# Kernel tuning notes

Hardware: AMD Instinct MI355X
Metric: run time of the kernel (lower is better)

## Reference

```python
import jax, jax.numpy as jnp
import numpy as np

L, D, DH, NH, P = 12, 768, 64, 12, 16
B, H_IMG, W_IMG = 16, 384, 384
MAX_GRID = 64


def setup_inputs() -> dict:
    key = jax.random.key(0)
    ks = jax.random.split(key, 10)
    r = lambda k, shp: (0.02 * jax.random.normal(k, shp, dtype=jnp.float32))
    return {
        "x": jax.random.normal(ks[0], (B, 3, H_IMG, W_IMG), dtype=jnp.float32),
        "conv_w": r(ks[1], (D, 3, P, P)),
        "conv_b": jnp.zeros((D,), jnp.float32),
        "ln_w": jnp.ones((D,), jnp.float32),
        "ln_b": jnp.zeros((D,), jnp.float32),
        "pos_y_emb": r(ks[2], (MAX_GRID, D)),
        "pos_x_emb": r(ks[3], (MAX_GRID, D)),
        "mha_ln_w": jnp.ones((L, D), jnp.float32),
        "mha_ln_b": jnp.zeros((L, D), jnp.float32),
        "qw": r(ks[4], (L, D, D)),
        "kw": r(ks[5], (L, D, D)),
        "vw": r(ks[6], (L, D, D)),
        "ffn_ln_w": jnp.ones((L, D), jnp.float32),
        "ffn_ln_b": jnp.zeros((L, D), jnp.float32),
        "w1": r(ks[7], (L, D, 4 * D)),
        "b1": jnp.zeros((L, 4 * D), jnp.float32),
        "w2": r(ks[8], (L, 4 * D, D)),
        "b2": jnp.zeros((L, D), jnp.float32),
        "x_shift": 0,
        "y_shift": 0,
    }


def _ln(x, w, b):
    m = jnp.mean(x, axis=-1, keepdims=True)
    v = jnp.var(x, axis=-1, keepdims=True)
    return (x - m) * jax.lax.rsqrt(v + 1e-5) * w + b


def reference(x, conv_w, conv_b, ln_w, ln_b, pos_y_emb, pos_x_emb,
              mha_ln_w, mha_ln_b, qw, kw, vw,
              ffn_ln_w, ffn_ln_b, w1, b1, w2, b2, x_shift, y_shift):
    # patch embed: conv + relu, to NHWC, layernorm
    h = jax.lax.conv_general_dilated(x, conv_w, (P, P), 'VALID',
                                     dimension_numbers=('NCHW', 'OIHW', 'NCHW'))
    h = jax.nn.relu(h + conv_b[None, :, None, None])
    h = jnp.transpose(h, (0, 2, 3, 1))  # [B, GH, GW, D]
    h = _ln(h, ln_w, ln_b)
    b, gh, gw, d = h.shape
    n = gh * gw
    # 2D factorized positional embedding, shared layernorm
    pos = (pos_y_emb[jnp.arange(gh) + y_shift][:, None, :]
           + pos_x_emb[jnp.arange(gw) + x_shift][None, :, :])  # [GH, GW, D]
    pos = _ln(pos, ln_w, ln_b).reshape(1, n, d)
    pos_emb = jnp.broadcast_to(pos, (b, n, d))
    t = h.reshape(b, n, d) + pos_emb
    scale = 1.0 / jnp.sqrt(jnp.float32(DH))
    for i in range(L):
        # pre-LN MHA (no output projection, mask=None / pretrain=False)
        tl = _ln(t, mha_ln_w[i], mha_ln_b[i])
        q = (tl @ qw[i]).reshape(b, n, NH, DH).transpose(0, 2, 1, 3)
        k = (tl @ kw[i]).reshape(b, n, NH, DH).transpose(0, 2, 1, 3)
        v = (tl @ vw[i]).reshape(b, n, NH, DH).transpose(0, 2, 1, 3)
        attn = jax.nn.softmax(jnp.einsum('bhqd,bhkd->bhqk', q, k) * scale, axis=-1)
        o = jnp.einsum('bhqk,bhkd->bhqd', attn, v).transpose(0, 2, 1, 3).reshape(b, n, d)
        t = t + o
        fl = _ln(t, ffn_ln_w[i], ffn_ln_b[i])
        t = t + (jax.nn.relu(fl @ w1[i] + b1[i]) @ w2[i] + b2[i])
    return t, pos_emb
```

## Files before the change

### kernel.cpp

```cpp
#include <hip/hip_runtime.h>

typedef unsigned short u16;
typedef __attribute__((ext_vector_type(4))) float f32x4;
typedef __attribute__((ext_vector_type(8))) short s16x8;

__device__ __forceinline__ u16 f2bf(float f) {
    union { float f; unsigned u; } v; v.f = f;
    unsigned r = v.u + 0x7FFFu + ((v.u >> 16) & 1u);
    return (u16)(r >> 16);
}

__device__ __forceinline__ void gload_lds16(const u16* g, u16* l) {
    __builtin_amdgcn_global_load_lds(
        (const __attribute__((address_space(1))) unsigned int*)(g),
        (__attribute__((address_space(3))) unsigned int*)(l),
        16, 0, 0);
}

#define NTOK 9216
#define SEQ  576
#define DMODEL 768
#define DFF  3072
#define NHEAD 12
#define HDIM 64

__global__ __launch_bounds__(256) void convert_bf16_kernel(const float* __restrict__ in,
                                                           u16* __restrict__ out, int n) {
    for (int i = blockIdx.x * 256 + threadIdx.x; i < n; i += gridDim.x * 256)
        out[i] = f2bf(in[i]);
}

__global__ __launch_bounds__(256) void copy_f32_kernel(const float* __restrict__ in,
                                                       float* __restrict__ out, int n4) {
    const float4* a = (const float4*)in;
    float4* o = (float4*)out;
    for (int i = blockIdx.x * 256 + threadIdx.x; i < n4; i += gridDim.x * 256)
        o[i] = a[i];
}

__global__ __launch_bounds__(256) void im2col_kernel(const float* __restrict__ x,
                                                     u16* __restrict__ out) {
    int tok = blockIdx.x;
    int b = tok / SEQ, n = tok % SEQ;
    int gy = n / 24, gx = n % 24;
    int tid = threadIdx.x;
#pragma unroll
    for (int j = 0; j < 3; ++j) {
        int col = tid + j * 256;
        int c = col >> 8, py = (col >> 4) & 15, px = col & 15;
        float v = x[(size_t)((b * 3 + c) * 384 + gy * 16 + py) * 384 + gx * 16 + px];
        out[(size_t)tok * DMODEL + col] = f2bf(v);
    }
}

__global__ __launch_bounds__(256) void transpose_layer_kernel(
        const float* __restrict__ qw, const float* __restrict__ kw, const float* __restrict__ vw,
        const float* __restrict__ w1, const float* __restrict__ w2,
        u16* __restrict__ wTq, u16* __restrict__ wTk, u16* __restrict__ wTv,
        u16* __restrict__ w1T, u16* __restrict__ w2T) {
    int bid = blockIdx.x;
    const float* src; u16* dst; int Kd, Nd, tile;
    if (bid < 1728)      { int m = bid / 576; src = m == 0 ? qw : (m == 1 ? kw : vw);
                           dst = m == 0 ? wTq : (m == 1 ? wTk : wTv); Kd = 768; Nd = 768; tile = bid % 576; }
    else if (bid < 4032) { src = w1; dst = w1T; Kd = 768; Nd = 3072; tile = bid - 1728; }
    else                 { src = w2; dst = w2T; Kd = 3072; Nd = 768; tile = bid - 4032; }
    int ntx = Nd / 32;
    int tk = (tile / ntx) * 32, tn = (tile % ntx) * 32;
    __shared__ float ts[32][33];
    int tx = threadIdx.x & 31, ty = threadIdx.x >> 5;
#pragma unroll
    for (int j = 0; j < 32; j += 8)
        ts[ty + j][tx] = src[(size_t)(tk + ty + j) * Nd + tn + tx];
    __syncthreads();
#pragma unroll
    for (int j = 0; j < 32; j += 8)
        dst[(size_t)(tn + ty + j) * Kd + tk + tx] = f2bf(ts[tx][ty + j]);
}

__global__ __launch_bounds__(256) void ln_bf16_kernel(const float* __restrict__ X,
                                                      const float* __restrict__ w,
                                                      const float* __restrict__ b,
                                                      u16* __restrict__ Y) {
    int row = blockIdx.x, tid = threadIdx.x;
    const float* x = X + (size_t)row * DMODEL;
    float v0 = x[tid], v1 = x[tid + 256], v2 = x[tid + 512];
    float s = v0 + v1 + v2, sq = v0 * v0 + v1 * v1 + v2 * v2;
#pragma unroll
    for (int off = 32; off >= 1; off >>= 1) { s += __shfl_down(s, off); sq += __shfl_down(sq, off); }
    __shared__ float red[8];
    if ((tid & 63) == 0) { red[tid >> 6] = s; red[4 + (tid >> 6)] = sq; }
    __syncthreads();
    float S = red[0] + red[1] + red[2] + red[3];
    float Q = red[4] + red[5] + red[6] + red[7];
    float mean = S * (1.f / DMODEL);
    float var = Q * (1.f / DMODEL) - mean * mean;
    float inv = rsqrtf(var + 1e-5f);
    u16* y = Y + (size_t)row * DMODEL;
    y[tid]       = f2bf((v0 - mean) * inv * w[tid]       + b[tid]);
    y[tid + 256] = f2bf((v1 - mean) * inv * w[tid + 256] + b[tid + 256]);
    y[tid + 512] = f2bf((v2 - mean) * inv * w[tid + 512] + b[tid + 512]);
}

__global__ __launch_bounds__(256) void ln_add_pos_kernel(float* __restrict__ T,
                                                         const float* __restrict__ w,
                                                         const float* __restrict__ b,
                                                         const float* __restrict__ posln) {
    int row = blockIdx.x, tid = threadIdx.x;
    float* x = T + (size_t)row * DMODEL;
    const float* p = posln + (size_t)(row % SEQ) * DMODEL;
    float v0 = x[tid], v1 = x[tid + 256], v2 = x[tid + 512];
    float s = v0 + v1 + v2, sq = v0 * v0 + v1 * v1 + v2 * v2;
#pragma unroll
    for (int off = 32; off >= 1; off >>= 1) { s += __shfl_down(s, off); sq += __shfl_down(sq, off); }
    __shared__ float red[8];
    if ((tid & 63) == 0) { red[tid >> 6] = s; red[4 + (tid >> 6)] = sq; }
    __syncthreads();
    float S = red[0] + red[1] + red[2] + red[3];
    float Q = red[4] + red[5] + red[6] + red[7];
    float mean = S * (1.f / DMODEL);
    float var = Q * (1.f / DMODEL) - mean * mean;
    float inv = rsqrtf(var + 1e-5f);
    x[tid]       = (v0 - mean) * inv * w[tid]       + b[tid]       + p[tid];
    x[tid + 256] = (v1 - mean) * inv * w[tid + 256] + b[tid + 256] + p[tid + 256];
    x[tid + 512] = (v2 - mean) * inv * w[tid + 512] + b[tid + 512] + p[tid + 512];
}

__global__ __launch_bounds__(256) void pos_ln_kernel(const float* __restrict__ py,
                                                     const float* __restrict__ px,
                                                     const float* __restrict__ w,
                                                     const float* __restrict__ b,
                                                     const int* __restrict__ xs_p,
                                                     const int* __restrict__ ys_p,
                                                     float* __restrict__ posln,
                                                     float* __restrict__ out2) {
    int row = blockIdx.x;
    int gy = row / 24, gx = row % 24;
    int ys = ys_p[0], xs = xs_p[0];
    int tid = threadIdx.x;
    float v[3]; float s = 0.f, sq = 0.f;
#pragma unroll
    for (int j = 0; j < 3; ++j) {
        int c = tid + j * 256;
        v[j] = py[(size_t)(gy + ys) * DMODEL + c] + px[(size_t)(gx + xs) * DMODEL + c];
        s += v[j]; sq += v[j] * v[j];
    }
#pragma unroll
    for (int off = 32; off >= 1; off >>= 1) { s += __shfl_down(s, off); sq += __shfl_down(sq, off); }
    __shared__ float red[8];
    if ((tid & 63) == 0) { red[tid >> 6] = s; red[4 + (tid >> 6)] = sq; }
    __syncthreads();
    float S = red[0] + red[1] + red[2] + red[3];
    float Q = red[4] + red[5] + red[6] + red[7];
    float mean = S * (1.f / DMODEL);
    float var = Q * (1.f / DMODEL) - mean * mean;
    float inv = rsqrtf(var + 1e-5f);
#pragma unroll
    for (int j = 0; j < 3; ++j) {
        int c = tid + j * 256;
        float y = (v[j] - mean) * inv * w[c] + b[c];
        posln[(size_t)row * DMODEL + c] = y;
        for (int bb = 0; bb < 16; ++bb)
            out2[((size_t)bb * SEQ + row) * DMODEL + c] = y;
    }
}

#define EPI_CONV 0
#define EPI_QKV  1
#define EPI_FFN1 3
#define EPI_FFN2 4

template <int EPI>
__global__ __launch_bounds__(256, 3) void gemm4w(const u16* __restrict__ A,
                                                 const u16* __restrict__ Bt,
                                                 float* __restrict__ outF,
                                                 u16* __restrict__ outB,
                                                 u16* __restrict__ outB2,
                                                 u16* __restrict__ outB3,
                                                 const float* __restrict__ bias,
                                                 int lda, int N, int K) {
    __shared__ __align__(16) u16 lds[3 * 8192];
    const int tid = threadIdx.x;
    const int wave = tid >> 6, lane = tid & 63;
    const int c_lo = lane & 15, c_hi = lane >> 4;
    const int wm = wave >> 1, wn = wave & 1;
    const int m0 = blockIdx.x * 128, n0 = blockIdx.y * 128;
    const int NT = K >> 5;

    const int srow = tid >> 2;
    const int koff = ((tid & 3) * 8) ^ (((tid >> 3) & 3) << 3);
    const u16* pA0 = A  + (size_t)(m0 + srow) * lda + koff;
    const u16* pA1 = pA0 + (size_t)64 * lda;
    const u16* pB0 = Bt + (size_t)(n0 + srow) * lda + koff;
    const u16* pB1 = pB0 + (size_t)64 * lda;
    f32x4 acc[4][4] = {};

    auto stage = [&](int t) {
        u16* buf = lds + (t % 3) * 8192;
        int k0 = t << 5;
        gload_lds16(pA0 + k0, buf + tid * 8);
        gload_lds16(pA1 + k0, buf + 2048 + tid * 8);
        gload_lds16(pB0 + k0, buf + 4096 + tid * 8);
        gload_lds16(pB1 + k0, buf + 6144 + tid * 8);
    };

    stage(0); stage(1);
    asm volatile("s_waitcnt vmcnt(4)" ::: "memory");
    __builtin_amdgcn_s_barrier();
    __builtin_amdgcn_sched_barrier(0);

    const int colA = (c_hi * 8) ^ (((c_lo >> 1) & 3) << 3);

    for (int t = 0; t < NT; ++t) {
        if (t + 2 < NT) stage(t + 2);
        const u16* buf = lds + (t % 3) * 8192;
        s16x8 af[4], bf[4];
#pragma unroll
        for (int m = 0; m < 4; ++m)
            af[m] = *(const s16x8*)(buf + (wm * 64 + m * 16 + c_lo) * 32 + colA);
#pragma unroll
        for (int n = 0; n < 4; ++n)
            bf[n] = *(const s16x8*)(buf + 4096 + (wn * 64 + n * 16 + c_lo) * 32 + colA);
        asm volatile("s_waitcnt lgkmcnt(0)" ::: "memory");
        __builtin_amdgcn_sched_barrier(0);
        __builtin_amdgcn_s_setprio(1);
#pragma unroll
        for (int m = 0; m < 4; ++m)
#pragma unroll
            for (int n = 0; n < 4; ++n)
                acc[m][n] = __builtin_amdgcn_mfma_f32_16x16x32_bf16(af[m], bf[n], acc[m][n], 0, 0, 0);
        __builtin_amdgcn_s_setprio(0);
        if (t + 2 < NT)      { asm volatile("s_waitcnt vmcnt(4)" ::: "memory"); }
        else if (t + 1 < NT) { asm volatile("s_waitcnt vmcnt(0)" ::: "memory"); }
        __builtin_amdgcn_s_barrier();
        __builtin_amdgcn_sched_barrier(0);
    }

#pragma unroll
    for (int mf = 0; mf < 4; ++mf)
#pragma unroll
        for (int nf = 0; nf < 4; ++nf)
#pragma unroll
            for (int rr = 0; rr < 4; ++rr) {
                int grow = m0 + wm * 64 + mf * 16 + c_hi * 4 + rr;
                int gcol = n0 + wn * 64 + nf * 16 + c_lo;
                float v = acc[mf][nf][rr];
                if (EPI == EPI_CONV) {
                    v += bias[gcol]; v = fmaxf(v, 0.f);
                    outF[(size_t)grow * 768 + gcol] = v;
                } else if (EPI == EPI_QKV) {
                    int sel = n0 / 768;
                    int lcol = gcol - sel * 768;
                    if (sel == 0)      outB [(size_t)grow * 768 + lcol] = f2bf(v);
                    else if (sel == 1) outB2[(size_t)grow * 768 + lcol] = f2bf(v);
                    else {
                        int b = grow / SEQ, nt = grow % SEQ;
                        int h = lcol >> 6, dh = lcol & 63;
                        outB3[(size_t)(((b * NHEAD + h) << 6) + dh) * SEQ + nt] = f2bf(v);
                    }
                } else if (EPI == EPI_FFN1) {
                    v += bias[gcol]; v = fmaxf(v, 0.f);
                    outB[(size_t)grow * N + gcol] = f2bf(v);
                } else if (EPI == EPI_FFN2) {
                    outF[(size_t)grow * 768 + gcol] += v + bias[gcol];
                }
            }
}

__global__ __launch_bounds__(256) void attn_kernel(const u16* __restrict__ Qb,
                                                   const u16* __restrict__ Kb,
                                                   const u16* __restrict__ Vt,
                                                   float* __restrict__ T) {
    int bid = blockIdx.x;
    int qt = bid / 192, bh = bid % 192;
    int b = bh / NHEAD, h = bh % NHEAD;
    int q0 = qt * 64;
    const int tid = threadIdx.x, wave = tid >> 6, lane = tid & 63;
    const int c_lo = lane & 15, c_hi = lane >> 4;
    __shared__ __align__(16) u16 Qs[64][72];
    __shared__ __align__(16) u16 Ks[64][72];
    __shared__ __align__(16) u16 Vs[64][72];
    __shared__ __align__(16) u16 Ps[4][16][72];
#pragma unroll
    for (int i = 0; i < 2; ++i) {
        int c = i * 256 + tid, row = c >> 3, slot = (c & 7) * 8;
        *(s16x8*)&Qs[row][slot] =
            *(const s16x8*)(Qb + ((size_t)(b * SEQ + q0 + row) * DMODEL + h * HDIM + slot));
    }
    s16x8 kreg[2], vreg[2];
    {
#pragma unroll
        for (int i = 0; i < 2; ++i) {
            int c = i * 256 + tid, row = c >> 3, slot = (c & 7) * 8;
            kreg[i] = *(const s16x8*)(Kb + ((size_t)(b * SEQ + row) * DMODEL + h * HDIM + slot));
            vreg[i] = *(const s16x8*)(Vt + ((size_t)((b * NHEAD + h) * HDIM + row) * SEQ + slot));
        }
    }
    f32x4 o[4] = {};
    float mrun[4], lrun[4];
#pragma unroll
    for (int r = 0; r < 4; ++r) { mrun[r] = -1e30f; lrun[r] = 0.f; }
    for (int t2 = 0; t2 < 9; ++t2) {
        __builtin_amdgcn_s_barrier();
#pragma unroll
        for (int i = 0; i < 2; ++i) {
            int c = i * 256 + tid, row = c >> 3, slot = (c & 7) * 8;
            *(s16x8*)&Ks[row][slot] = kreg[i];
            *(s16x8*)&Vs[row][slot] = vreg[i];
        }
        asm volatile("s_waitcnt lgkmcnt(0)" ::: "memory");
        __builtin_amdgcn_s_barrier();
        __builtin_amdgcn_sched_barrier(0);
        if (t2 < 8) {
            int kv0 = (t2 + 1) * 64;
#pragma unroll
            for (int i = 0; i < 2; ++i) {
                int c = i * 256 + tid, row = c >> 3, slot = (c & 7) * 8;
                kreg[i] = *(const s16x8*)(Kb + ((size_t)(b * SEQ + kv0 + row) * DMODEL + h * HDIM + slot));
                vreg[i] = *(const s16x8*)(Vt + ((size_t)((b * NHEAD + h) * HDIM + row) * SEQ + kv0 + slot));
            }
        }
        f32x4 s[4] = {};
        s16x8 aq[2];
#pragma unroll
        for (int ks = 0; ks < 2; ++ks)
            aq[ks] = *(const s16x8*)&Qs[wave * 16 + c_lo][ks * 32 + c_hi * 8];
#pragma unroll
        for (int nf = 0; nf < 4; ++nf)
#pragma unroll
            for (int ks = 0; ks < 2; ++ks) {
                s16x8 bk = *(const s16x8*)&Ks[nf * 16 + c_lo][ks * 32 + c_hi * 8];
                s[nf] = __builtin_amdgcn_mfma_f32_16x16x32_bf16(aq[ks], bk, s[nf], 0, 0, 0);
            }
#pragma unroll
        for (int nf = 0; nf < 4; ++nf)
#pragma unroll
            for (int r = 0; r < 4; ++r) s[nf][r] *= 0.125f;
        float mx[4];
#pragma unroll
        for (int r = 0; r < 4; ++r)
            mx[r] = fmaxf(fmaxf(s[0][r], s[1][r]), fmaxf(s[2][r], s[3][r]));
#pragma unroll
        for (int off = 1; off < 16; off <<= 1)
#pragma unroll
            for (int r = 0; r < 4; ++r) mx[r] = fmaxf(mx[r], __shfl_xor(mx[r], off));
        float alpha[4];
#pragma unroll
        for (int r = 0; r < 4; ++r) {
            float mn = fmaxf(mrun[r], mx[r]);
            alpha[r] = __expf(mrun[r] - mn);
            mrun[r] = mn;
            lrun[r] *= alpha[r];
        }
        float ls[4] = {0.f, 0.f, 0.f, 0.f};
        u16 pb[4][4];
#pragma unroll
        for (int nf = 0; nf < 4; ++nf)
#pragma unroll
            for (int r = 0; r < 4; ++r) {
                float p = __expf(s[nf][r] - mrun[r]);
                ls[r] += p;
                pb[nf][r] = f2bf(p);
            }
#pragma unroll
        for (int off = 1; off < 16; off <<= 1)
#pragma unroll
            for (int r = 0; r < 4; ++r) ls[r] += __shfl_xor(ls[r], off);
#pragma unroll
        for (int r = 0; r < 4; ++r) lrun[r] += ls[r];
#pragma unroll
        for (int df = 0; df < 4; ++df)
#pragma unroll
            for (int r = 0; r < 4; ++r) o[df][r] *= alpha[r];
#pragma unroll
        for (int nf = 0; nf < 4; ++nf)
#pragma unroll
            for (int r = 0; r < 4; ++r)
                Ps[wave][c_hi * 4 + r][c_lo + nf * 16] = pb[nf][r];
        asm volatile("s_waitcnt lgkmcnt(0)" ::: "memory");
        s16x8 pa[2];
#pragma unroll
        for (int ks = 0; ks < 2; ++ks)
            pa[ks] = *(const s16x8*)&Ps[wave][c_lo][ks * 32 + c_hi * 8];
#pragma unroll
        for (int df = 0; df < 4; ++df)
#pragma unroll
            for (int ks = 0; ks < 2; ++ks) {
                s16x8 bv = *(const s16x8*)&Vs[df * 16 + c_lo][ks * 32 + c_hi * 8];
                o[df] = __builtin_amdgcn_mfma_f32_16x16x32_bf16(pa[ks], bv, o[df], 0, 0, 0);
            }
    }
#pragma unroll
    for (int df = 0; df < 4; ++df)
#pragma unroll
        for (int r = 0; r < 4; ++r) {
            int grow = b * SEQ + q0 + wave * 16 + c_hi * 4 + r;
            int gcol = h * HDIM + df * 16 + c_lo;
            T[(size_t)grow * DMODEL + gcol] += o[df][r] / lrun[r];
        }
}

extern "C" void kernel_launch(void* const* d_in, const int* in_sizes, int n_in,
                              void* d_out, int out_size, void* d_ws, size_t ws_size,
                              hipStream_t stream) {
    (void)in_sizes; (void)n_in; (void)out_size; (void)ws_size;
    const float* x        = (const float*)d_in[0];
    const float* conv_w   = (const float*)d_in[1];
    const float* conv_b   = (const float*)d_in[2];
    const float* ln_w     = (const float*)d_in[3];
    const float* ln_b     = (const float*)d_in[4];
    const float* pos_y    = (const float*)d_in[5];
    const float* pos_x    = (const float*)d_in[6];
    const float* mha_ln_w = (const float*)d_in[7];
    const float* mha_ln_b = (const float*)d_in[8];
    const float* qw       = (const float*)d_in[9];
    const float* kw       = (const float*)d_in[10];
    const float* vw       = (const float*)d_in[11];
    const float* ffn_ln_w = (const float*)d_in[12];
    const float* ffn_ln_b = (const float*)d_in[13];
    const float* w1       = (const float*)d_in[14];
    const float* b1       = (const float*)d_in[15];
    const float* w2       = (const float*)d_in[16];
    const float* b2       = (const float*)d_in[17];
    const int*   xs       = (const int*)d_in[18];
    const int*   ys       = (const int*)d_in[19];
    float* out1 = (float*)d_out;
    float* out2 = out1 + (size_t)NTOK * DMODEL;

    size_t off = 0;
    char* ws = (char*)d_ws;
    auto carve = [&](size_t bytes) { char* p = ws + off; off += (bytes + 255) & ~(size_t)255; return p; };
    u16* wTqkv = (u16*)carve((size_t)3 * 768 * 768 * 2);
    u16* w1T = (u16*)carve((size_t)DFF * DMODEL * 2);
    u16* w2T = (u16*)carve((size_t)DMODEL * DFF * 2);
    float* t  = (float*)carve((size_t)NTOK * DMODEL * 4);
    u16* tl   = (u16*)carve((size_t)NTOK * DMODEL * 2);
    u16* qb   = (u16*)carve((size_t)NTOK * DMODEL * 2);
    u16* kb   = (u16*)carve((size_t)NTOK * DMODEL * 2);
    u16* vT   = (u16*)carve((size_t)NTOK * DMODEL * 2);
    u16* hb   = (u16*)carve((size_t)NTOK * DFF * 2);
    float* posln = (float*)carve((size_t)SEQ * DMODEL * 4);
    u16* wTq = wTqkv;
    u16* wTk = wTqkv + (size_t)768 * 768;
    u16* wTv = wTqkv + (size_t)2 * 768 * 768;
    u16* cw   = wTqkv;
    u16* im2c = hb;

    convert_bf16_kernel<<<1152, 256, 0, stream>>>(conv_w, cw, 768 * 768);
    im2col_kernel<<<NTOK, 256, 0, stream>>>(x, im2c);
    gemm4w<EPI_CONV><<<dim3(72, 6), 256, 0, stream>>>(im2c, cw, t, nullptr, nullptr, nullptr,
                                                      conv_b, 768, 768, 768);
    pos_ln_kernel<<<SEQ, 256, 0, stream>>>(pos_y, pos_x, ln_w, ln_b, xs, ys, posln, out2);
    ln_add_pos_kernel<<<NTOK, 256, 0, stream>>>(t, ln_w, ln_b, posln);

    for (int i = 0; i < 12; ++i) {
        transpose_layer_kernel<<<6336, 256, 0, stream>>>(
            qw + (size_t)i * 768 * 768, kw + (size_t)i * 768 * 768, vw + (size_t)i * 768 * 768,
            w1 + (size_t)i * 768 * DFF, w2 + (size_t)i * DFF * 768,
            wTq, wTk, wTv, w1T, w2T);
        ln_bf16_kernel<<<NTOK, 256, 0, stream>>>(t, mha_ln_w + i * DMODEL, mha_ln_b + i * DMODEL, tl);
        gemm4w<EPI_QKV><<<dim3(72, 18), 256, 0, stream>>>(tl, wTqkv, nullptr, qb, kb, vT,
                                                          nullptr, 768, 2304, 768);
        attn_kernel<<<16 * NHEAD * 9, 256, 0, stream>>>(qb, kb, vT, t);
        ln_bf16_kernel<<<NTOK, 256, 0, stream>>>(t, ffn_ln_w + i * DMODEL, ffn_ln_b + i * DMODEL, tl);
        gemm4w<EPI_FFN1><<<dim3(72, 24), 256, 0, stream>>>(tl, w1T, nullptr, hb, nullptr, nullptr,
                                                           b1 + (size_t)i * DFF, 768, 3072, 768);
        gemm4w<EPI_FFN2><<<dim3(72, 6), 256, 0, stream>>>(hb, w2T, t, nullptr, nullptr, nullptr,
                                                          b2 + (size_t)i * DMODEL, 3072, 768, 3072);
    }
    copy_f32_kernel<<<2048, 256, 0, stream>>>(t, out1, (NTOK * DMODEL) / 4);
}
```

Before: 3.260 ms.

## Single-buffer GEMM main loop and use 64x64 vectorized weight transpose

```diff
diff --git a/kernel.cpp b/kernel.cpp
--- a/kernel.cpp
+++ b/kernel.cpp
@@ -53,28 +53,38 @@
     }
 }
 
-__global__ __launch_bounds__(256) void transpose_layer_kernel(
+__global__ __launch_bounds__(256) void transpose64_kernel(
         const float* __restrict__ qw, const float* __restrict__ kw, const float* __restrict__ vw,
         const float* __restrict__ w1, const float* __restrict__ w2,
         u16* __restrict__ wTq, u16* __restrict__ wTk, u16* __restrict__ wTv,
         u16* __restrict__ w1T, u16* __restrict__ w2T) {
     int bid = blockIdx.x;
     const float* src; u16* dst; int Kd, Nd, tile;
-    if (bid < 1728)      { int m = bid / 576; src = m == 0 ? qw : (m == 1 ? kw : vw);
-                           dst = m == 0 ? wTq : (m == 1 ? wTk : wTv); Kd = 768; Nd = 768; tile = bid % 576; }
-    else if (bid < 4032) { src = w1; dst = w1T; Kd = 768; Nd = 3072; tile = bid - 1728; }
-    else                 { src = w2; dst = w2T; Kd = 3072; Nd = 768; tile = bid - 4032; }
-    int ntx = Nd / 32;
-    int tk = (tile / ntx) * 32, tn = (tile % ntx) * 32;
-    __shared__ float ts[32][33];
-    int tx = threadIdx.x & 31, ty = threadIdx.x >> 5;
-#pragma unroll
-    for (int j = 0; j < 32; j += 8)
-        ts[ty + j][tx] = src[(size_t)(tk + ty + j) * Nd + tn + tx];
+    if (bid < 432)       { int m = bid / 144; src = m == 0 ? qw : (m == 1 ? kw : vw);
+                           dst = m == 0 ? wTq : (m == 1 ? wTk : wTv); Kd = 768; Nd = 768; tile = bid % 144; }
+    else if (bid < 1008) { src = w1; dst = w1T; Kd = 768; Nd = 3072; tile = bid - 432; }
+    else                 { src = w2; dst = w2T; Kd = 3072; Nd = 768; tile = bid - 1008; }
+    int ntx = Nd >> 6;
+    int tk = (tile / ntx) << 6, tn = (tile % ntx) << 6;
+    __shared__ float ts[64][65];
+    int tx4 = threadIdx.x & 15, ty = threadIdx.x >> 4;
+#pragma unroll
+    for (int j = 0; j < 64; j += 16) {
+        float4 v = *(const float4*)&src[(size_t)(tk + ty + j) * Nd + tn + tx4 * 4];
+        ts[ty + j][tx4 * 4 + 0] = v.x;
+        ts[ty + j][tx4 * 4 + 1] = v.y;
+        ts[ty + j][tx4 * 4 + 2] = v.z;
+        ts[ty + j][tx4 * 4 + 3] = v.w;
+    }
     __syncthreads();
-#pragma unroll
-    for (int j = 0; j < 32; j += 8)
-        dst[(size_t)(tn + ty + j) * Kd + tk + tx] = f2bf(ts[tx][ty + j]);
+    int kx = threadIdx.x & 31, ry = threadIdx.x >> 5;
+#pragma unroll
+    for (int j = 0; j < 64; j += 8) {
+        int r = ry + j;
+        unsigned lo = f2bf(ts[2 * kx][r]);
+        unsigned hi = f2bf(ts[2 * kx + 1][r]);
+        *(unsigned*)&dst[(size_t)(tn + r) * Kd + tk + 2 * kx] = lo | (hi << 16);
+    }
 }
 
 __global__ __launch_bounds__(256) void ln_bf16_kernel(const float* __restrict__ X,
@@ -170,7 +180,7 @@
 #define EPI_FFN2 4
 
 template <int EPI>
-__global__ __launch_bounds__(256, 3) void gemm4w(const u16* __restrict__ A,
+__global__ __launch_bounds__(256, 3) void gemm97(const u16* __restrict__ A,
                                                  const u16* __restrict__ Bt,
                                                  float* __restrict__ outF,
                                                  u16* __restrict__ outB,
@@ -178,7 +188,7 @@
                                                  u16* __restrict__ outB3,
                                                  const float* __restrict__ bias,
                                                  int lda, int N, int K) {
-    __shared__ __align__(16) u16 lds[3 * 8192];
+    __shared__ __align__(16) u16 lds[8192];
     const int tid = threadIdx.x;
     const int wave = tid >> 6, lane = tid & 63;
     const int c_lo = lane & 15, c_hi = lane >> 4;
@@ -194,45 +204,28 @@
     const u16* pB1 = pB0 + (size_t)64 * lda;
     f32x4 acc[4][4] = {};
 
-    auto stage = [&](int t) {
-        u16* buf = lds + (t % 3) * 8192;
+    const int colA = (c_hi * 8) ^ (((c_lo >> 1) & 3) << 3);
+
+    for (int t = 0; t < NT; ++t) {
         int k0 = t << 5;
-        gload_lds16(pA0 + k0, buf + tid * 8);
-        gload_lds16(pA1 + k0, buf + 2048 + tid * 8);
-        gload_lds16(pB0 + k0, buf + 4096 + tid * 8);
-        gload_lds16(pB1 + k0, buf + 6144 + tid * 8);
-    };
-
-    stage(0); stage(1);
-    asm volatile("s_waitcnt vmcnt(4)" ::: "memory");
-    __builtin_amdgcn_s_barrier();
-    __builtin_amdgcn_sched_barrier(0);
-
-    const int colA = (c_hi * 8) ^ (((c_lo >> 1) & 3) << 3);
-
-    for (int t = 0; t < NT; ++t) {
-        if (t + 2 < NT) stage(t + 2);
-        const u16* buf = lds + (t % 3) * 8192;
+        __syncthreads();
+        gload_lds16(pA0 + k0, lds + tid * 8);
+        gload_lds16(pA1 + k0, lds + 2048 + tid * 8);
+        gload_lds16(pB0 + k0, lds + 4096 + tid * 8);
+        gload_lds16(pB1 + k0, lds + 6144 + tid * 8);
+        __syncthreads();
         s16x8 af[4], bf[4];
 #pragma unroll
         for (int m = 0; m < 4; ++m)
-            af[m] = *(const s16x8*)(buf + (wm * 64 + m * 16 + c_lo) * 32 + colA);
+            af[m] = *(const s16x8*)(lds + (wm * 64 + m * 16 + c_lo) * 32 + colA);
 #pragma unroll
         for (int n = 0; n < 4; ++n)
-            bf[n] = *(const s16x8*)(buf + 4096 + (wn * 64 + n * 16 + c_lo) * 32 + colA);
-        asm volatile("s_waitcnt lgkmcnt(0)" ::: "memory");
-        __builtin_amdgcn_sched_barrier(0);
-        __builtin_amdgcn_s_setprio(1);
+            bf[n] = *(const s16x8*)(lds + 4096 + (wn * 64 + n * 16 + c_lo) * 32 + colA);
 #pragma unroll
         for (int m = 0; m < 4; ++m)
 #pragma unroll
             for (int n = 0; n < 4; ++n)
                 acc[m][n] = __builtin_amdgcn_mfma_f32_16x16x32_bf16(af[m], bf[n], acc[m][n], 0, 0, 0);
-        __builtin_amdgcn_s_setprio(0);
-        if (t + 2 < NT)      { asm volatile("s_waitcnt vmcnt(4)" ::: "memory"); }
-        else if (t + 1 < NT) { asm volatile("s_waitcnt vmcnt(0)" ::: "memory"); }
-        __builtin_amdgcn_s_barrier();
-        __builtin_amdgcn_sched_barrier(0);
     }
 
 #pragma unroll
@@ -447,24 +440,24 @@
 
     convert_bf16_kernel<<<1152, 256, 0, stream>>>(conv_w, cw, 768 * 768);
     im2col_kernel<<<NTOK, 256, 0, stream>>>(x, im2c);
-    gemm4w<EPI_CONV><<<dim3(72, 6), 256, 0, stream>>>(im2c, cw, t, nullptr, nullptr, nullptr,
+    gemm97<EPI_CONV><<<dim3(72, 6), 256, 0, stream>>>(im2c, cw, t, nullptr, nullptr, nullptr,
                                                       conv_b, 768, 768, 768);
     pos_ln_kernel<<<SEQ, 256, 0, stream>>>(pos_y, pos_x, ln_w, ln_b, xs, ys, posln, out2);
     ln_add_pos_kernel<<<NTOK, 256, 0, stream>>>(t, ln_w, ln_b, posln);
 
     for (int i = 0; i < 12; ++i) {
-        transpose_layer_kernel<<<6336, 256, 0, stream>>>(
+        transpose64_kernel<<<1584, 256, 0, stream>>>(
             qw + (size_t)i * 768 * 768, kw + (size_t)i * 768 * 768, vw + (size_t)i * 768 * 768,
             w1 + (size_t)i * 768 * DFF, w2 + (size_t)i * DFF * 768,
             wTq, wTk, wTv, w1T, w2T);
         ln_bf16_kernel<<<NTOK, 256, 0, stream>>>(t, mha_ln_w + i * DMODEL, mha_ln_b + i * DMODEL, tl);
-        gemm4w<EPI_QKV><<<dim3(72, 18), 256, 0, stream>>>(tl, wTqkv, nullptr, qb, kb, vT,
+        gemm97<EPI_QKV><<<dim3(72, 18), 256, 0, stream>>>(tl, wTqkv, nullptr, qb, kb, vT,
                                                           nullptr, 768, 2304, 768);
         attn_kernel<<<16 * NHEAD * 9, 256, 0, stream>>>(qb, kb, vT, t);
         ln_bf16_kernel<<<NTOK, 256, 0, stream>>>(t, ffn_ln_w + i * DMODEL, ffn_ln_b + i * DMODEL, tl);
-        gemm4w<EPI_FFN1><<<dim3(72, 24), 256, 0, stream>>>(tl, w1T, nullptr, hb, nullptr, nullptr,
+        gemm97<EPI_FFN1><<<dim3(72, 24), 256, 0, stream>>>(tl, w1T, nullptr, hb, nullptr, nullptr,
                                                            b1 + (size_t)i * DFF, 768, 3072, 768);
-        gemm4w<EPI_FFN2><<<dim3(72, 6), 256, 0, stream>>>(hb, w2T, t, nullptr, nullptr, nullptr,
+        gemm97<EPI_FFN2><<<dim3(72, 6), 256, 0, stream>>>(hb, w2T, t, nullptr, nullptr, nullptr,
                                                           b2 + (size_t)i * DMODEL, 3072, 768, 3072);
     }
     copy_f32_kernel<<<2048, 256, 0, stream>>>(t, out1, (NTOK * DMODEL) / 4);
```

Measured after the change: 3.383 ms. 3.8% more time.
